# Kernel optimization log

Measured on AMD Instinct MI355X. Metric: run time of the kernel, lower is better.

## Reference

```python
import jax, jax.numpy as jnp
import numpy as np

B = 32          # batch_size
M = 1024        # mesh_num (nodes per sub-graph)
D_IN = 128      # sub_node_feature_input_dim
D_OUT = 128     # sub_node_feature_output_dim
E_DIM = 64      # embedding dim per node


def setup_inputs() -> dict:
    key = jax.random.key(0)
    k1, k2, k3, k4 = jax.random.split(key, 4)
    return {
        "node_feature_group": jax.random.normal(k1, (B * M, D_IN), dtype=jnp.float32),
        "embedding_group": jax.random.normal(k2, (B * M, E_DIM), dtype=jnp.float32),
        "W1": jax.random.normal(k3, (D_OUT, D_IN), dtype=jnp.float32) * (1.0 / np.sqrt(D_IN)),
        "W2": jax.random.normal(k4, (D_OUT, D_OUT), dtype=jnp.float32) * (1.0 / np.sqrt(D_OUT)),
    }


def reference(node_feature_group, embedding_group, W1, W2):
    # The torch module builds a (B*M)x(B*M) block-diagonal adjacency via
    # torch.block_diag; off-block entries are exactly zero, and row sums /
    # D^-1/2 A D^-1/2 normalization act per block, so we compute per-graph.
    E = embedding_group.reshape(B, M, E_DIM)
    adj = jnp.maximum(jnp.einsum('bme,bne->bmn', E, E), 0.0)  # clamp(E E^T, 0)
    adj = adj + jnp.eye(M, dtype=adj.dtype)                   # A = adj + I
    d = adj.sum(-1)                                           # [B, M]
    dinv = d ** -0.5                                          # symmetric=True
    dad = dinv[:, :, None] * adj * dinv[:, None, :]           # D^-1/2 A D^-1/2

    X = node_feature_group.reshape(B, M, D_IN)
    y = jax.nn.relu(jnp.einsum('bmn,bnd->bmd', dad, X) @ W1.T)   # gcn1
    y = jax.nn.relu(jnp.einsum('bmn,bnd->bmd', dad, y) @ W2.T)   # gcn2
    # Dropout is identity in eval mode.
    return y.reshape(B * M, D_OUT)
```

## Files before the change

kernel.cpp:

```cpp
#include <hip/hip_runtime.h>
#include <stdint.h>

#define B_  32
#define M_  1024
#define DF  128
#define ED  64

typedef __attribute__((ext_vector_type(8))) short short8;
typedef __attribute__((ext_vector_type(4))) short short4v;
typedef __attribute__((ext_vector_type(4))) float floatx4;

__device__ inline unsigned short f2bf(float f) {
    union { float f; unsigned u; } v; v.f = f;
    unsigned r = v.u + 0x7fffu + ((v.u >> 16) & 1u);
    return (unsigned short)(r >> 16);
}

__device__ inline short8 cvt8(float4 a, float4 b) {
    short8 s;
    s[0] = (short)f2bf(a.x); s[1] = (short)f2bf(a.y);
    s[2] = (short)f2bf(a.z); s[3] = (short)f2bf(a.w);
    s[4] = (short)f2bf(b.x); s[5] = (short)f2bf(b.y);
    s[6] = (short)f2bf(b.z); s[7] = (short)f2bf(b.w);
    return s;
}

__device__ inline void load_lds16(const void* g, void* l) {
    __builtin_amdgcn_global_load_lds(
        (const __attribute__((address_space(1))) unsigned int*)g,
        (__attribute__((address_space(3))) unsigned int*)l, 16, 0, 0);
}

#define SWZ(colb, row) ((colb) ^ (((row) & 7) << 4))

__device__ inline void remap_block(int& b, int& mt2) {
    int lin = blockIdx.y * 16 + blockIdx.x;
    int g = lin & 7, kk = lin >> 3;
    b = g * 4 + (kk >> 4);
    mt2 = kk & 15;
}

__global__ __launch_bounds__(256) void prep_kernel(
    const float* __restrict__ E, const float* __restrict__ X,
    unsigned short* __restrict__ Ebf, float* __restrict__ dinv,
    unsigned short* __restrict__ Xt) {
    int b, mt2; remap_block(b, mt2);
    int m0 = mt2 * 64;
    int t = threadIdx.x;
    int w = t >> 6, lane = t & 63, quad = lane >> 4, lc = lane & 15;

    __shared__ unsigned short sEn[128 * 72];
    __shared__ float sDinv[64];

    const float* Eb = E + (size_t)b * M_ * ED;
    unsigned short* Ebg = Ebf + (size_t)b * M_ * ED;
    int base_m = m0 + w * 16;

    short8 afr[2];
    for (int ks = 0; ks < 2; ++ks) {
        const float* p = Eb + (size_t)(base_m + lc) * ED + ks * 32 + quad * 8;
        afr[ks] = cvt8(*(const float4*)p, *(const float4*)(p + 4));
    }
    floatx4 rsum = (floatx4){0.f, 0.f, 0.f, 0.f};

    for (int nc = 0; nc < 8; ++nc) {
        __syncthreads();
        for (int it = 0; it < 4; ++it) {
            int c = t + 256 * it;
            int row = c >> 3, off = (c & 7) * 8;
            const float* p = Eb + (size_t)(nc * 128 + row) * ED + off;
            *(short8*)(&sEn[row * 72 + off]) = cvt8(*(const float4*)p, *(const float4*)(p + 4));
        }
        __syncthreads();
        if ((mt2 & 7) == nc) {
            int half = mt2 >> 3;
            for (int it = 0; it < 2; ++it) {
                int c = t + 256 * it;
                int row = half * 64 + (c >> 3), off = (c & 7) * 8;
                *(short8*)(Ebg + (size_t)(nc * 128 + row) * ED + off) =
                    *(const short8*)(&sEn[row * 72 + off]);
            }
        }
        for (int nt = 0; nt < 8; ++nt) {
            short8 b0 = *(const short8*)(&sEn[(nt * 16 + lc) * 72 + quad * 8]);
            short8 b1 = *(const short8*)(&sEn[(nt * 16 + lc) * 72 + 32 + quad * 8]);
            floatx4 s = (floatx4){0.f, 0.f, 0.f, 0.f};
            s = __builtin_amdgcn_mfma_f32_16x16x32_bf16(afr[0], b0, s, 0, 0, 0);
            s = __builtin_amdgcn_mfma_f32_16x16x32_bf16(afr[1], b1, s, 0, 0, 0);
            int n = nc * 128 + nt * 16 + lc;
            for (int r = 0; r < 4; ++r) {
                int m = base_m + quad * 4 + r;
                float v = fmaxf(s[r], 0.f);
                if (m == n) v += 1.0f;
                rsum[r] += v;
            }
        }
    }
    for (int r = 0; r < 4; ++r) {
        float v = rsum[r];
        v += __shfl_xor(v, 1, 16);
        v += __shfl_xor(v, 2, 16);
        v += __shfl_xor(v, 4, 16);
        v += __shfl_xor(v, 8, 16);
        if (lc == 0) {
            float dvv = rsqrtf(v);
            int mloc = w * 16 + quad * 4 + r;
            sDinv[mloc] = dvv;
            dinv[b * M_ + m0 + mloc] = dvv;
        }
    }
    __syncthreads();
    {
        int nloc = t >> 5;
        int d4 = (t & 31) * 4;
        for (int pass = 0; pass < 8; ++pass) {
            int n = pass * 8 + nloc;
            float sc = sDinv[n];
            float4 v = *(const float4*)(X + (size_t)(b * M_ + m0 + n) * DF + d4);
            sEn[(d4 + 0) * 72 + n] = f2bf(v.x * sc);
            sEn[(d4 + 1) * 72 + n] = f2bf(v.y * sc);
            sEn[(d4 + 2) * 72 + n] = f2bf(v.z * sc);
            sEn[(d4 + 3) * 72 + n] = f2bf(v.w * sc);
        }
    }
    __syncthreads();
    for (int it = 0; it < 4; ++it) {
        int c = t + 256 * it;
        int d = c >> 3, off = (c & 7) * 8;
        *(short8*)(Xt + (size_t)(b * DF + d) * M_ + m0 + off) =
            *(const short8*)(&sEn[d * 72 + off]);
    }
}

template <int MODE>
__global__ __launch_bounds__(512, 2) void layer_kernel(
    const unsigned short* __restrict__ Ebf,
    const unsigned short* __restrict__ Pt,
    const float* __restrict__ Wf,
    const float* __restrict__ dinv,
    unsigned short* __restrict__ OutT,
    float* __restrict__ OutF) {
    int b = blockIdx.x, mt = blockIdx.y;
    int m0 = mt * 128;
    int t = threadIdx.x;
    int w = t >> 6, lane = t & 63, quad = lane >> 4, lc = lane & 15;
    int wr = w >> 1, wc = w & 1;

    __shared__ char lds[131072];

    const unsigned short* Eb = Ebf + (size_t)b * M_ * ED;
    const unsigned short* Pb = Pt + (size_t)b * DF * M_;

    short8 ae[2][2];
    for (int i = 0; i < 2; ++i) {
        int row = m0 + wr * 32 + i * 16 + lc;
        for (int ks = 0; ks < 2; ++ks)
            ae[i][ks] = *(const short8*)(Eb + (size_t)row * ED + ks * 32 + quad * 8);
    }
    float dv[2][4];
    for (int i = 0; i < 2; ++i)
        for (int r = 0; r < 4; ++r)
            dv[i][r] = dinv[b * M_ + m0 + wr * 32 + i * 16 + quad * 4 + r];

    floatx4 acc[2][4];
    for (int i = 0; i < 2; ++i)
        for (int j = 0; j < 4; ++j) acc[i][j] = (floatx4){0.f, 0.f, 0.f, 0.f};

    int srcColE = ((lane & 7) ^ (lane >> 3)) * 8;
    int srcColP = ((lane & 15) ^ ((w & 1) * 4 + (lane >> 4))) * 8;
    auto stage = [&](int sel, int nc) {
        for (int r = 0; r < 2; ++r) {
            int slot = r * 8 + w;
            int row = slot * 8 + (lane >> 3);
            const void* gp = Eb + (size_t)(nc * 128 + row) * ED + srcColE;
            load_lds16(gp, lds + sel * 16384 + slot * 1024);
        }
        for (int r = 0; r < 4; ++r) {
            int slot = r * 8 + w;
            int row = slot * 4 + (lane >> 4);
            const void* gp = Pb + (size_t)row * M_ + nc * 128 + srcColP;
            load_lds16(gp, lds + 65536 + sel * 32768 + slot * 1024);
        }
    };

    int cur = 0;
    stage(0, 0);
    __syncthreads();

    for (int nc = 0; nc < 8; ++nc) {
        if (nc < 7) stage(cur ^ 1, nc + 1);
        const char* sEnB = lds + cur * 16384;
        const char* sPWB = lds + 65536 + cur * 32768;
        char* sSB = lds + 32768;
        for (int jt = 0; jt < 4; ++jt) {
            int ncol = wc * 64 + jt * 16;
            int nrow = ncol + lc;
            short8 b0 = *(const short8*)(sEnB + nrow * 128 + SWZ(quad * 16, nrow));
            short8 b1 = *(const short8*)(sEnB + nrow * 128 + SWZ(64 + quad * 16, nrow));
            for (int i = 0; i < 2; ++i) {
                floatx4 s = (floatx4){0.f, 0.f, 0.f, 0.f};
                s = __builtin_amdgcn_mfma_f32_16x16x32_bf16(ae[i][0], b0, s, 0, 0, 0);
                s = __builtin_amdgcn_mfma_f32_16x16x32_bf16(ae[i][1], b1, s, 0, 0, 0);
                int mloc = wr * 32 + i * 16 + quad * 4;
                for (int r = 0; r < 4; ++r) {
                    float v = fmaxf(s[r], 0.f);
                    if (m0 + mloc + r == nc * 128 + ncol + lc) v += 1.0f;
                    int mrow = mloc + r;
                    *(unsigned short*)(sSB + mrow * 256 + SWZ(2 * (ncol + lc), mrow)) = f2bf(v);
                }
            }
        }
        __syncthreads();
        for (int ks = 0; ks < 4; ++ks) {
            short8 afr[2], bfr[4];
            for (int i = 0; i < 2; ++i) {
                int row = wr * 32 + i * 16 + lc;
                afr[i] = *(const short8*)(sSB + row * 256 + SWZ(ks * 64 + quad * 16, row));
            }
            for (int j = 0; j < 4; ++j) {
                int row = wc * 64 + j * 16 + lc;
                bfr[j] = *(const short8*)(sPWB + row * 256 + SWZ(ks * 64 + quad * 16, row));
            }
            for (int i = 0; i < 2; ++i)
                for (int j = 0; j < 4; ++j)
                    acc[i][j] = __builtin_amdgcn_mfma_f32_16x16x32_bf16(afr[i], bfr[j], acc[i][j], 0, 0, 0);
        }
        __syncthreads();
        cur ^= 1;
    }

    char* sYB = lds + 32768;
    char* sWB = lds + 65536;
    for (int i = 0; i < 2; ++i)
        for (int j = 0; j < 4; ++j) {
            int mloc = wr * 32 + i * 16 + quad * 4;
            int col = wc * 64 + j * 16 + lc;
            for (int r = 0; r < 4; ++r) {
                int mrow = mloc + r;
                *(unsigned short*)(sYB + mrow * 256 + SWZ(2 * col, mrow)) =
                    f2bf(acc[i][j][r] * dv[i][r]);
            }
        }
    for (int it = 0; it < 4; ++it) {
        int c = t + 512 * it;
        int row = c >> 4, colb = (c & 15) * 16;
        const float* p = Wf + row * DF + (c & 15) * 8;
        *(short8*)(sWB + row * 256 + SWZ(colb, row)) =
            cvt8(*(const float4*)p, *(const float4*)(p + 4));
    }
    __syncthreads();
    floatx4 accH[2][4];
    for (int i = 0; i < 2; ++i)
        for (int j = 0; j < 4; ++j) accH[i][j] = (floatx4){0.f, 0.f, 0.f, 0.f};
    for (int ks = 0; ks < 4; ++ks) {
        short8 afr[2], bfr[4];
        for (int i = 0; i < 2; ++i) {
            int row = wr * 32 + i * 16 + lc;
            afr[i] = *(const short8*)(sYB + row * 256 + SWZ(ks * 64 + quad * 16, row));
        }
        for (int j = 0; j < 4; ++j) {
            int row = wc * 64 + j * 16 + lc;
            bfr[j] = *(const short8*)(sWB + row * 256 + SWZ(ks * 64 + quad * 16, row));
        }
        for (int i = 0; i < 2; ++i)
            for (int j = 0; j < 4; ++j)
                accH[i][j] = __builtin_amdgcn_mfma_f32_16x16x32_bf16(afr[i], bfr[j], accH[i][j], 0, 0, 0);
    }
    if (MODE == 2) {
        __syncthreads();
        float* sF = (float*)lds;
        for (int i = 0; i < 2; ++i)
            for (int j = 0; j < 4; ++j) {
                int mrow = wr * 32 + i * 16 + quad * 4;
                int col = wc * 64 + j * 16 + lc;
                for (int r = 0; r < 4; ++r)
                    sF[(mrow + r) * 132 + col] = fmaxf(accH[i][j][r], 0.f);
            }
        __syncthreads();
        float* Ob = OutF + ((size_t)b * M_ + m0) * DF;
        for (int it = 0; it < 8; ++it) {
            int c = t + 512 * it;
            int row = c >> 5, off = (c & 31) * 4;
            *(float4*)(Ob + (size_t)row * DF + off) = *(const float4*)(&sF[row * 132 + off]);
        }
    } else {
        __syncthreads();
        unsigned short* sT = (unsigned short*)lds;
        for (int i = 0; i < 2; ++i)
            for (int j = 0; j < 4; ++j) {
                int mrow = wr * 32 + i * 16 + quad * 4;
                int col = wc * 64 + j * 16 + lc;
                short4v pk;
                for (int r = 0; r < 4; ++r)
                    pk[r] = (short)f2bf(fmaxf(accH[i][j][r], 0.f) * dv[i][r]);
                *(short4v*)(&sT[col * 136 + mrow]) = pk;
            }
        __syncthreads();
        for (int it = 0; it < 4; ++it) {
            int c = t + 512 * it;
            int o = c >> 4, off = (c & 15) * 8;
            *(short8*)(OutT + (size_t)(b * DF + o) * M_ + m0 + off) =
                *(const short8*)(&sT[o * 136 + off]);
        }
    }
}

__global__ __launch_bounds__(256) void cast_kernel(
    const float* __restrict__ E, const float* __restrict__ W1,
    const float* __restrict__ W2, unsigned short* __restrict__ Ebf,
    unsigned short* __restrict__ W1bf, unsigned short* __restrict__ W2bf) {
    const int NE = B_ * M_ * ED;
    const int NW = DF * DF;
    int idx = (blockIdx.x * 256 + threadIdx.x) * 4;
    const float* src; unsigned short* dst; int off;
    if (idx < NE)            { src = E;  dst = Ebf;  off = idx; }
    else if (idx < NE + NW)  { src = W1; dst = W1bf; off = idx - NE; }
    else                     { src = W2; dst = W2bf; off = idx - NE - NW; }
    float4 v = *(const float4*)(src + off);
    ushort4 o;
    o.x = f2bf(v.x); o.y = f2bf(v.y); o.z = f2bf(v.z); o.w = f2bf(v.w);
    *(ushort4*)(dst + off) = o;
}

__global__ __launch_bounds__(256) void degree_kernel(
    const unsigned short* __restrict__ Ebf, float* __restrict__ dinv) {
    int mt = blockIdx.x, b = blockIdx.y;
    int t = threadIdx.x;
    int w = t >> 6, lane = t & 63, quad = lane >> 4, lc = lane & 15;
    __shared__ unsigned short sEn[128][72];
    const unsigned short* Eb = Ebf + (size_t)b * M_ * ED;
    short8 afr[2][2];
    for (int i = 0; i < 2; ++i) {
        int row = mt * 128 + w * 32 + i * 16 + lc;
        for (int ks = 0; ks < 2; ++ks)
            afr[i][ks] = *(const short8*)(Eb + (size_t)row * ED + ks * 32 + quad * 8);
    }
    floatx4 rsum[2];
    rsum[0] = (floatx4){0.f,0.f,0.f,0.f};
    rsum[1] = (floatx4){0.f,0.f,0.f,0.f};
    for (int nc = 0; nc < 8; ++nc) {
        __syncthreads();
        for (int it = 0; it < 4; ++it) {
            int c = t + 256 * it;
            int row = c >> 3, off = (c & 7) * 8;
            *(short8*)(&sEn[row][off]) =
                *(const short8*)(Eb + (size_t)(nc * 128 + row) * ED + off);
        }
        __syncthreads();
        for (int nt = 0; nt < 8; ++nt) {
            short8 b0 = *(const short8*)(&sEn[nt * 16 + lc][quad * 8]);
            short8 b1 = *(const short8*)(&sEn[nt * 16 + lc][32 + quad * 8]);
            for (int i = 0; i < 2; ++i) {
                floatx4 s = (floatx4){0.f,0.f,0.f,0.f};
                s = __builtin_amdgcn_mfma_f32_16x16x32_bf16(afr[i][0], b0, s, 0, 0, 0);
                s = __builtin_amdgcn_mfma_f32_16x16x32_bf16(afr[i][1], b1, s, 0, 0, 0);
                for (int r = 0; r < 4; ++r) rsum[i][r] += fmaxf(s[r], 0.f);
            }
        }
    }
    for (int i = 0; i < 2; ++i)
        for (int r = 0; r < 4; ++r) {
            float v = rsum[i][r];
            v += __shfl_xor(v, 1, 16);
            v += __shfl_xor(v, 2, 16);
            v += __shfl_xor(v, 4, 16);
            v += __shfl_xor(v, 8, 16);
            if (lc == 0) {
                int row = mt * 128 + w * 32 + i * 16 + quad * 4 + r;
                dinv[b * M_ + row] = rsqrtf(1.0f + v);
            }
        }
}

__global__ __launch_bounds__(256) void tscale128_kernel(
    const float* __restrict__ X, const float* __restrict__ dinv,
    unsigned short* __restrict__ Xt) {
    int mt = blockIdx.x, b = blockIdx.y;
    int t = threadIdx.x;
    __shared__ unsigned short sT[128][136];
    int nloc = t >> 5;
    int d4 = (t & 31) * 4;
    for (int pass = 0; pass < 16; ++pass) {
        int n = pass * 8 + nloc;
        int grow = b * M_ + mt * 128 + n;
        float sc = dinv[grow];
        float4 v = *(const float4*)(X + (size_t)grow * DF + d4);
        sT[d4 + 0][n] = f2bf(v.x * sc);
        sT[d4 + 1][n] = f2bf(v.y * sc);
        sT[d4 + 2][n] = f2bf(v.z * sc);
        sT[d4 + 3][n] = f2bf(v.w * sc);
    }
    __syncthreads();
    for (int it = 0; it < 8; ++it) {
        int c = t + 256 * it;
        int d = c >> 4, off = (c & 15) * 8;
        *(short8*)(Xt + (size_t)(b * DF + d) * M_ + mt * 128 + off) =
            *(const short8*)(&sT[d][off]);
    }
}

template <int MODE>
__global__ __launch_bounds__(256) void gcn_kernel(
    const unsigned short* __restrict__ Ebf,
    const unsigned short* __restrict__ Pt,
    const unsigned short* __restrict__ Wbf,
    const float* __restrict__ dinv,
    unsigned short* __restrict__ OutT,
    float* __restrict__ OutF) {
    int mt = blockIdx.x, b = blockIdx.y;
    int t = threadIdx.x;
    int w = t >> 6, lane = t & 63, quad = lane >> 4, lc = lane & 15;
    int wr = w & 1, wc = w >> 1;
    __shared__ unsigned short sEn[128][72];
    __shared__ unsigned short sS[128][136];
    __shared__ unsigned short sPW[128][136];
    const unsigned short* Eb = Ebf + (size_t)b * M_ * ED;
    short8 ae[4][2];
    for (int i = 0; i < 4; ++i) {
        int row = mt * 128 + wr * 64 + i * 16 + lc;
        for (int ks = 0; ks < 2; ++ks)
            ae[i][ks] = *(const short8*)(Eb + (size_t)row * ED + ks * 32 + quad * 8);
    }
    floatx4 accZ[4][4];
    for (int i = 0; i < 4; ++i)
        for (int j = 0; j < 4; ++j) accZ[i][j] = (floatx4){0.f,0.f,0.f,0.f};
    for (int nc = 0; nc < 8; ++nc) {
        __syncthreads();
        for (int it = 0; it < 4; ++it) {
            int c = t + 256 * it;
            int row = c >> 3, off = (c & 7) * 8;
            *(short8*)(&sEn[row][off]) =
                *(const short8*)(Eb + (size_t)(nc * 128 + row) * ED + off);
        }
        for (int it = 0; it < 8; ++it) {
            int c = t + 256 * it;
            int drow = c >> 4, off = (c & 15) * 8;
            *(short8*)(&sPW[drow][off]) =
                *(const short8*)(Pt + (size_t)(b * DF + drow) * M_ + nc * 128 + off);
        }
        __syncthreads();
        for (int jt = 0; jt < 4; ++jt) {
            int ncol = wc * 64 + jt * 16;
            short8 b0 = *(const short8*)(&sEn[ncol + lc][quad * 8]);
            short8 b1 = *(const short8*)(&sEn[ncol + lc][32 + quad * 8]);
            for (int i = 0; i < 4; ++i) {
                floatx4 s = (floatx4){0.f,0.f,0.f,0.f};
                s = __builtin_amdgcn_mfma_f32_16x16x32_bf16(ae[i][0], b0, s, 0, 0, 0);
                s = __builtin_amdgcn_mfma_f32_16x16x32_bf16(ae[i][1], b1, s, 0, 0, 0);
                int mrow = wr * 64 + i * 16 + quad * 4;
                for (int r = 0; r < 4; ++r) {
                    float v = fmaxf(s[r], 0.f);
                    if (mt == nc && (mrow + r) == (ncol + lc)) v += 1.0f;
                    sS[mrow + r][ncol + lc] = f2bf(v);
                }
            }
        }
        __syncthreads();
        for (int ks = 0; ks < 4; ++ks) {
            short8 afr[4];
            for (int i = 0; i < 4; ++i)
                afr[i] = *(const short8*)(&sS[wr * 64 + i * 16 + lc][ks * 32 + quad * 8]);
            for (int j = 0; j < 4; ++j) {
                short8 bfr = *(const short8*)(&sPW[wc * 64 + j * 16 + lc][ks * 32 + quad * 8]);
                for (int i = 0; i < 4; ++i)
                    accZ[i][j] = __builtin_amdgcn_mfma_f32_16x16x32_bf16(afr[i], bfr, accZ[i][j], 0, 0, 0);
            }
        }
    }
    float dv[4][4];
    for (int i = 0; i < 4; ++i)
        for (int r = 0; r < 4; ++r)
            dv[i][r] = dinv[b * M_ + mt * 128 + wr * 64 + i * 16 + quad * 4 + r];
    __syncthreads();
    for (int i = 0; i < 4; ++i)
        for (int j = 0; j < 4; ++j) {
            int mrow = wr * 64 + i * 16 + quad * 4;
            int col = wc * 64 + j * 16 + lc;
            for (int r = 0; r < 4; ++r)
                sS[mrow + r][col] = f2bf(accZ[i][j][r] * dv[i][r]);
        }
    for (int it = 0; it < 8; ++it) {
        int c = t + 256 * it;
        int row = c >> 4, off = (c & 15) * 8;
        *(short8*)(&sPW[row][off]) = *(const short8*)(Wbf + row * DF + off);
    }
    __syncthreads();
    floatx4 accH[4][4];
    for (int i = 0; i < 4; ++i)
        for (int j = 0; j < 4; ++j) accH[i][j] = (floatx4){0.f,0.f,0.f,0.f};
    for (int ks = 0; ks < 4; ++ks) {
        short8 afr[4], bfr[4];
        for (int i = 0; i < 4; ++i)
            afr[i] = *(const short8*)(&sS[wr * 64 + i * 16 + lc][ks * 32 + quad * 8]);
        for (int j = 0; j < 4; ++j)
            bfr[j] = *(const short8*)(&sPW[wc * 64 + j * 16 + lc][ks * 32 + quad * 8]);
        for (int i = 0; i < 4; ++i)
            for (int j = 0; j < 4; ++j)
                accH[i][j] = __builtin_amdgcn_mfma_f32_16x16x32_bf16(afr[i], bfr[j], accH[i][j], 0, 0, 0);
    }
    if (MODE == 2) {
        float* Ob = OutF + ((size_t)b * M_ + mt * 128) * DF;
        for (int i = 0; i < 4; ++i)
            for (int j = 0; j < 4; ++j) {
                int mrow = wr * 64 + i * 16 + quad * 4;
                int col = wc * 64 + j * 16 + lc;
                for (int r = 0; r < 4; ++r)
                    Ob[(size_t)(mrow + r) * DF + col] = fmaxf(accH[i][j][r], 0.f);
            }
    } else {
        __syncthreads();
        for (int i = 0; i < 4; ++i)
            for (int j = 0; j < 4; ++j) {
                int mrow = wr * 64 + i * 16 + quad * 4;
                int col = wc * 64 + j * 16 + lc;
                for (int r = 0; r < 4; ++r)
                    sS[col][mrow + r] = f2bf(fmaxf(accH[i][j][r], 0.f) * dv[i][r]);
            }
        __syncthreads();
        unsigned short* Ob = OutT + (size_t)b * DF * M_ + mt * 128;
        for (int it = 0; it < 8; ++it) {
            int c = t + 256 * it;
            int orow = c >> 4, off = (c & 15) * 8;
            *(short8*)(Ob + (size_t)orow * M_ + off) = *(const short8*)(&sS[orow][off]);
        }
    }
}

extern "C" void kernel_launch(void* const* d_in, const int* in_sizes, int n_in,
                              void* d_out, int out_size, void* d_ws, size_t ws_size,
                              hipStream_t stream) {
    (void)in_sizes; (void)n_in; (void)out_size;
    const float* X  = (const float*)d_in[0];
    const float* E  = (const float*)d_in[1];
    const float* W1 = (const float*)d_in[2];
    const float* W2 = (const float*)d_in[3];
    float* out = (float*)d_out;

    char* ws = (char*)d_ws;
    unsigned short* Ebf  = (unsigned short*)(ws);
    unsigned short* W1bf = (unsigned short*)(ws + 4194304);
    unsigned short* W2bf = (unsigned short*)(ws + 4227072);
    float*          dinv = (float*)(ws + 4259840);
    unsigned short* Xt   = (unsigned short*)(ws + 4390912);
    unsigned short* Ht   = (unsigned short*)(ws + 12779520);
    const size_t NEED = 21168128ull;

    if (ws_size >= NEED) {
        prep_kernel<<<dim3(16, 32), 256, 0, stream>>>(E, X, Ebf, dinv, Xt);
        layer_kernel<1><<<dim3(32, 8), 512, 0, stream>>>(Ebf, Xt, W1, dinv, Ht, nullptr);
        layer_kernel<2><<<dim3(32, 8), 512, 0, stream>>>(Ebf, Ht, W2, dinv, nullptr, out);
    } else {
        cast_kernel<<<2080, 256, 0, stream>>>(E, W1, W2, Ebf, W1bf, W2bf);
        degree_kernel<<<dim3(8, 32), 256, 0, stream>>>(Ebf, dinv);
        tscale128_kernel<<<dim3(8, 32), 256, 0, stream>>>(X, dinv, Xt);
        gcn_kernel<1><<<dim3(8, 32), 256, 0, stream>>>(Ebf, Xt, W1bf, dinv, Ht, nullptr);
        gcn_kernel<2><<<dim3(8, 32), 256, 0, stream>>>(Ebf, Ht, W2bf, dinv, nullptr, out);
    }
}
```

Baseline: 144.5 us.

## Enlarge prep tiles, register-prefetch embedding chunks, use LDS-only barriers

The prep kernel now handles 128 rows per block with 512 threads on a 32x8 grid, which halves the number of times each graph's embeddings are re-read and converted. The next embedding chunk is prefetched into registers while the current chunk is processed. A custom barrier that waits only on LDS counters replaces __syncthreads in the prep loop and at one point in the layer kernel, so pending global loads are not drained at each barrier. This adds register pressure and depends on correct waitcnt handling, which makes the synchronisation fragile.

```diff
diff --git a/kernel.cpp b/kernel.cpp
--- a/kernel.cpp
+++ b/kernel.cpp
@@ -31,26 +31,27 @@
         (__attribute__((address_space(3))) unsigned int*)l, 16, 0, 0);
 }
 
+__device__ inline void barrier_lds_only() {
+    asm volatile("s_waitcnt lgkmcnt(0)" ::: "memory");
+    __builtin_amdgcn_sched_barrier(0);
+    __builtin_amdgcn_s_barrier();
+    __builtin_amdgcn_sched_barrier(0);
+}
+
 #define SWZ(colb, row) ((colb) ^ (((row) & 7) << 4))
 
-__device__ inline void remap_block(int& b, int& mt2) {
-    int lin = blockIdx.y * 16 + blockIdx.x;
-    int g = lin & 7, kk = lin >> 3;
-    b = g * 4 + (kk >> 4);
-    mt2 = kk & 15;
-}
-
-__global__ __launch_bounds__(256) void prep_kernel(
+
+__global__ __launch_bounds__(512) void prep_kernel(
     const float* __restrict__ E, const float* __restrict__ X,
     unsigned short* __restrict__ Ebf, float* __restrict__ dinv,
     unsigned short* __restrict__ Xt) {
-    int b, mt2; remap_block(b, mt2);
-    int m0 = mt2 * 64;
+    int b = blockIdx.x, mt = blockIdx.y;
+    int m0 = mt * 128;
     int t = threadIdx.x;
     int w = t >> 6, lane = t & 63, quad = lane >> 4, lc = lane & 15;
 
-    __shared__ unsigned short sEn[128 * 72];
-    __shared__ float sDinv[64];
+    __shared__ unsigned short sBuf[128 * 136];
+    __shared__ float sDinv[128];
 
     const float* Eb = E + (size_t)b * M_ * ED;
     unsigned short* Ebg = Ebf + (size_t)b * M_ * ED;
@@ -63,27 +64,35 @@
     }
     floatx4 rsum = (floatx4){0.f, 0.f, 0.f, 0.f};
 
+    float4 pre[4];
+    auto ldreg = [&](int nc) {
+        for (int it = 0; it < 2; ++it) {
+            int c = t + 512 * it;
+            const float* p = Eb + (size_t)(nc * 128 + (c >> 3)) * ED + (c & 7) * 8;
+            pre[it * 2]     = *(const float4*)p;
+            pre[it * 2 + 1] = *(const float4*)(p + 4);
+        }
+    };
+    ldreg(0);
+
     for (int nc = 0; nc < 8; ++nc) {
-        __syncthreads();
-        for (int it = 0; it < 4; ++it) {
-            int c = t + 256 * it;
-            int row = c >> 3, off = (c & 7) * 8;
-            const float* p = Eb + (size_t)(nc * 128 + row) * ED + off;
-            *(short8*)(&sEn[row * 72 + off]) = cvt8(*(const float4*)p, *(const float4*)(p + 4));
-        }
-        __syncthreads();
-        if ((mt2 & 7) == nc) {
-            int half = mt2 >> 3;
+        for (int it = 0; it < 2; ++it) {
+            int c = t + 512 * it;
+            *(short8*)(&sBuf[(c >> 3) * 72 + (c & 7) * 8]) = cvt8(pre[it * 2], pre[it * 2 + 1]);
+        }
+        if (nc < 7) ldreg(nc + 1);
+        barrier_lds_only();
+        if (mt == nc) {
             for (int it = 0; it < 2; ++it) {
-                int c = t + 256 * it;
-                int row = half * 64 + (c >> 3), off = (c & 7) * 8;
+                int c = t + 512 * it;
+                int row = c >> 3, off = (c & 7) * 8;
                 *(short8*)(Ebg + (size_t)(nc * 128 + row) * ED + off) =
-                    *(const short8*)(&sEn[row * 72 + off]);
+                    *(const short8*)(&sBuf[row * 72 + off]);
             }
         }
         for (int nt = 0; nt < 8; ++nt) {
-            short8 b0 = *(const short8*)(&sEn[(nt * 16 + lc) * 72 + quad * 8]);
-            short8 b1 = *(const short8*)(&sEn[(nt * 16 + lc) * 72 + 32 + quad * 8]);
+            short8 b0 = *(const short8*)(&sBuf[(nt * 16 + lc) * 72 + quad * 8]);
+            short8 b1 = *(const short8*)(&sBuf[(nt * 16 + lc) * 72 + 32 + quad * 8]);
             floatx4 s = (floatx4){0.f, 0.f, 0.f, 0.f};
             s = __builtin_amdgcn_mfma_f32_16x16x32_bf16(afr[0], b0, s, 0, 0, 0);
             s = __builtin_amdgcn_mfma_f32_16x16x32_bf16(afr[1], b1, s, 0, 0, 0);
@@ -95,6 +104,7 @@
                 rsum[r] += v;
             }
         }
+        barrier_lds_only();
     }
     for (int r = 0; r < 4; ++r) {
         float v = rsum[r];
@@ -114,21 +124,21 @@
         int nloc = t >> 5;
         int d4 = (t & 31) * 4;
         for (int pass = 0; pass < 8; ++pass) {
-            int n = pass * 8 + nloc;
+            int n = pass * 16 + nloc;
             float sc = sDinv[n];
             float4 v = *(const float4*)(X + (size_t)(b * M_ + m0 + n) * DF + d4);
-            sEn[(d4 + 0) * 72 + n] = f2bf(v.x * sc);
-            sEn[(d4 + 1) * 72 + n] = f2bf(v.y * sc);
-            sEn[(d4 + 2) * 72 + n] = f2bf(v.z * sc);
-            sEn[(d4 + 3) * 72 + n] = f2bf(v.w * sc);
+            sBuf[(d4 + 0) * 136 + n] = f2bf(v.x * sc);
+            sBuf[(d4 + 1) * 136 + n] = f2bf(v.y * sc);
+            sBuf[(d4 + 2) * 136 + n] = f2bf(v.z * sc);
+            sBuf[(d4 + 3) * 136 + n] = f2bf(v.w * sc);
         }
     }
     __syncthreads();
     for (int it = 0; it < 4; ++it) {
-        int c = t + 256 * it;
-        int d = c >> 3, off = (c & 7) * 8;
+        int c = t + 512 * it;
+        int d = c >> 4, off = (c & 15) * 8;
         *(short8*)(Xt + (size_t)(b * DF + d) * M_ + m0 + off) =
-            *(const short8*)(&sEn[d * 72 + off]);
+            *(const short8*)(&sBuf[d * 136 + off]);
     }
 }
 
@@ -210,7 +220,7 @@
                 }
             }
         }
-        __syncthreads();
+        barrier_lds_only();
         for (int ks = 0; ks < 4; ++ks) {
             short8 afr[2], bfr[4];
             for (int i = 0; i < 2; ++i) {
@@ -546,7 +556,7 @@
     const size_t NEED = 21168128ull;
 
     if (ws_size >= NEED) {
-        prep_kernel<<<dim3(16, 32), 256, 0, stream>>>(E, X, Ebf, dinv, Xt);
+        prep_kernel<<<dim3(32, 8), 512, 0, stream>>>(E, X, Ebf, dinv, Xt);
         layer_kernel<1><<<dim3(32, 8), 512, 0, stream>>>(Ebf, Xt, W1, dinv, Ht, nullptr);
         layer_kernel<2><<<dim3(32, 8), 512, 0, stream>>>(Ebf, Ht, W2, dinv, nullptr, out);
     } else {
```

Result: faster. 141.6 us (-2.0%).
